# Performance work log

Hardware: AMD Instinct MI355X
Metric: run time of the kernel (lower is better)

## Reference

```python
import jax, jax.numpy as jnp
import numpy as np

HIDDEN = 1024
HEADS = 16
HEAD_DIM = HIDDEN // HEADS


def setup_inputs() -> dict:
    key = jax.random.key(0)
    ks = jax.random.split(key, 9)
    s = 1.0 / np.sqrt(HIDDEN)
    return {
        "x": jax.random.normal(ks[0], (2, 2048, HIDDEN), dtype=jnp.float32),
        "Wq": jax.random.uniform(ks[1], (HIDDEN, HIDDEN), jnp.float32, -s, s),
        "bq": jax.random.uniform(ks[2], (HIDDEN,), jnp.float32, -s, s),
        "Wk": jax.random.uniform(ks[3], (HIDDEN, HIDDEN), jnp.float32, -s, s),
        "bk": jax.random.uniform(ks[4], (HIDDEN,), jnp.float32, -s, s),
        "Wv": jax.random.uniform(ks[5], (HIDDEN, HIDDEN), jnp.float32, -s, s),
        "bv": jax.random.uniform(ks[6], (HIDDEN,), jnp.float32, -s, s),
        "Wo": jax.random.uniform(ks[7], (HIDDEN, HIDDEN), jnp.float32, -s, s),
        "bo": jax.random.uniform(ks[8], (HIDDEN,), jnp.float32, -s, s),
    }


def reference(x, Wq, bq, Wk, bk, Wv, bv, Wo, bo):
    B, N, C = x.shape
    H, D = HEADS, HEAD_DIM
    # torch Linear: y = x @ W.T + b; weights here stored as (out, in)
    q = (x @ Wq.T + bq).reshape(B, N, H, D).transpose(0, 2, 1, 3)  # bhnd
    k = (x @ Wk.T + bk).reshape(B, N, H, D).transpose(0, 2, 1, 3)
    v = (x @ Wv.T + bv).reshape(B, N, H, D).transpose(0, 2, 1, 3)
    scale = D ** -0.5
    attn = jnp.einsum("bhnd,bhmd->bhnm", q, k) * scale
    attn = jax.nn.softmax(attn, axis=-1)
    out = jnp.einsum("bhnm,bhmd->bhnd", attn, v)
    out = out.transpose(0, 2, 1, 3).reshape(B, N, C)
    return out @ Wo.T + bo
```

## Files before the change

### kernel.cpp

```cpp
#include <hip/hip_runtime.h>
#include <stdint.h>

#define HIDDEN 1024
#define HEADS 16
#define HEAD_DIM 64
#define NBATCH 2
#define SEQ 2048

typedef short bh8 __attribute__((ext_vector_type(8)));
typedef _Float16 hf4 __attribute__((ext_vector_type(4)));
typedef _Float16 hf8 __attribute__((ext_vector_type(8)));
typedef float fx4 __attribute__((ext_vector_type(4)));

#define MFMA_BF16(a, b, c) __builtin_amdgcn_mfma_f32_16x16x32_bf16((a), (b), (c), 0, 0, 0)
#define MFMA_F16_16(a, b, c) __builtin_amdgcn_mfma_f32_16x16x16f16((a), (b), (c), 0, 0, 0)

__device__ __forceinline__ short f2bf(float f) {
  union { float f; uint32_t u; } v; v.f = f;
  uint32_t r = v.u + 0x7fffu + ((v.u >> 16) & 1u);
  return (short)(r >> 16);
}
__device__ __forceinline__ short f2h(float f) {
  union { _Float16 h; short s; } v; v.h = (_Float16)f;
  return v.s;
}

typedef __attribute__((address_space(1))) void GV;
typedef __attribute__((address_space(3))) void LV;
__device__ __forceinline__ void gl_lds16(const void* g, void* l) {
  __builtin_amdgcn_global_load_lds((GV*)g, (LV*)l, 16, 0, 0);
}

__device__ __forceinline__ size_t img_off(int row, int k) {
  int rt = row >> 7, kt = k >> 6;
  int g = (((row & 127) >> 4) << 1) + ((k & 63) >> 5);
  int l = (((k & 31) >> 3) << 4) + (row & 15);
  return ((size_t)((rt * 16 + kt) * 16 + g) << 9) + (l << 3) + (k & 7);
}

__global__ void cvt_kernel(const float* __restrict__ x,
                           const float* __restrict__ wq, const float* __restrict__ wk,
                           const float* __restrict__ wv, const float* __restrict__ wo,
                           short* __restrict__ xb, short* __restrict__ wqb,
                           short* __restrict__ wkb, short* __restrict__ wvb,
                           short* __restrict__ wob) {
  long t = (long)blockIdx.x * blockDim.x + threadIdx.x;
  long i = t * 4;
  const float* s; short* d; long off;
  if (i < 4194304L) { s = x; d = xb; off = i; }
  else {
    long j = i - 4194304L;
    int w = (int)(j >> 20);
    off = j & 1048575L;
    s = (w == 0) ? wq : (w == 1) ? wk : (w == 2) ? wv : wo;
    d = (w == 0) ? wqb : (w == 1) ? wkb : (w == 2) ? wvb : wob;
  }
  float4 v = *(const float4*)(s + off);
  short4 o;
  o.x = f2bf(v.x); o.y = f2bf(v.y); o.z = f2bf(v.z); o.w = f2bf(v.w);
  int row = (int)(off >> 10), k = (int)(off & 1023);
  *(short4*)(d + img_off(row, k)) = o;
}

__global__ __launch_bounds__(256)
void qkv_kernel(const short* __restrict__ xb,
                const short* __restrict__ wqb, const short* __restrict__ wkb,
                const short* __restrict__ wvb,
                const float* __restrict__ bq, const float* __restrict__ bk,
                const float* __restrict__ bv,
                short* __restrict__ Q, short* __restrict__ K, short* __restrict__ Vt) {
  __shared__ __align__(16) short Alds[8192];
  __shared__ __align__(16) short Blds[8192];
  const int z = blockIdx.z;
  const short* W = (z == 0) ? wqb : (z == 1) ? wkb : wvb;
  const float* bias = (z == 0) ? bq : (z == 1) ? bk : bv;
  const int mt = blockIdx.y;
  const int ot = blockIdx.x;
  const int tid = threadIdx.x;
  const int lane = tid & 63, w = tid >> 6;
  const int r = lane & 15, q = lane >> 4;
  const int wr = w >> 1, wc = w & 1;

  fx4 acc[4][4] = {};

  for (int kt = 0; kt < 16; ++kt) {
#pragma unroll
    for (int i = 0; i < 4; ++i) {
      int c = w * 4 + i;
      gl_lds16(xb + (((size_t)(mt * 16 + kt) * 16 + c) << 9) + lane * 8,
               (char*)Alds + c * 1024);
      gl_lds16(W + (((size_t)(ot * 16 + kt) * 16 + c) << 9) + lane * 8,
               (char*)Blds + c * 1024);
    }
    __syncthreads();
#pragma unroll
    for (int ks = 0; ks < 2; ++ks) {
      bh8 af[4], bf_[4];
#pragma unroll
      for (int ti = 0; ti < 4; ++ti)
        af[ti] = *(const bh8*)&Alds[(((wr * 4 + ti) * 2 + ks) << 9) + lane * 8];
#pragma unroll
      for (int tj = 0; tj < 4; ++tj)
        bf_[tj] = *(const bh8*)&Blds[(((wc * 4 + tj) * 2 + ks) << 9) + lane * 8];
#pragma unroll
      for (int ti = 0; ti < 4; ++ti)
#pragma unroll
        for (int tj = 0; tj < 4; ++tj)
          acc[ti][tj] = MFMA_BF16(af[ti], bf_[tj], acc[ti][tj]);
    }
    __syncthreads();
  }

  const float QS = 0.18033688011112042f;
#pragma unroll
  for (int ti = 0; ti < 4; ++ti)
#pragma unroll
    for (int tj = 0; tj < 4; ++tj)
#pragma unroll
      for (int i = 0; i < 4; ++i) {
        int row = mt * 128 + wr * 64 + ti * 16 + q * 4 + i;
        int col = ot * 128 + wc * 64 + tj * 16 + r;
        float v = acc[ti][tj][i] + bias[col];
        int b = row >> 11, n = row & 2047;
        int h = col >> 6, d = col & 63;
        int bh = b * 16 + h;
        size_t base = (size_t)bh * 131072;
        if (z == 0) {
          Q[base + (size_t)n * 64 + d] = f2bf(v * QS);
        } else if (z == 1) {
          int jj = n >> 7, rin = n & 127;
          int g = ((rin >> 4) * 2) + (d >> 5);
          int lp = (((d & 31) >> 3) * 16) + (rin & 15);
          K[base + jj * 8192 + g * 512 + lp * 8 + (d & 7)] = f2bf(v);
        } else {
          int jj = n >> 7, keyin = n & 127;
          int dt = d >> 4, rp = d & 15;
          int ks2 = keyin >> 4, pi = ks2 >> 1, hh = ks2 & 1;
          int qp = (keyin & 15) >> 2, ii = keyin & 3;
          Vt[base + jj * 8192 + (dt * 4 + pi) * 512 + (qp * 16 + rp) * 8 + hh * 4 + ii] = f2h(v);
        }
      }
}

__global__ __launch_bounds__(512, 4)
void attn_kernel(const short* __restrict__ Q, const short* __restrict__ Kf,
                 const short* __restrict__ Vf, short* __restrict__ A) {
  __shared__ __align__(16) short Klds[8192];
  __shared__ __align__(16) short Vlds[8192];

  const int tid = threadIdx.x;
  const int lane = tid & 63, w = tid >> 6;
  const int r = lane & 15, q = lane >> 4;
  const int n0 = blockIdx.x * 128;
  const int bh = blockIdx.y;

  const short* Qg = Q + (size_t)bh * 131072;
  const short* Kg = Kf + (size_t)bh * 131072;
  const short* Vg = Vf + (size_t)bh * 131072;

  bh8 qf[2];
#pragma unroll
  for (int ks = 0; ks < 2; ++ks)
    qf[ks] = *(const bh8*)(Qg + (size_t)(n0 + w * 16 + r) * 64 + ks * 32 + q * 8);

  fx4 o[4] = {};
  float l_run = 0.f;

  for (int j = 0; j < 16; ++j) {
    const short* kt = Kg + j * 8192;
    const short* vt = Vg + j * 8192;
#pragma unroll
    for (int i = 0; i < 4; ++i) {
      if (w < 4) {
        int c = w * 4 + i;
        gl_lds16(kt + c * 512 + lane * 8, (char*)Klds + c * 1024);
      } else {
        int c = (w - 4) * 4 + i;
        gl_lds16(vt + c * 512 + lane * 8, (char*)Vlds + c * 1024);
      }
    }
    __syncthreads();

    fx4 s[8] = {};
#pragma unroll
    for (int ks = 0; ks < 2; ++ks)
#pragma unroll
      for (int tj = 0; tj < 8; ++tj) {
        bh8 kf = *(const bh8*)&Klds[(tj * 2 + ks) * 512 + lane * 8];
        s[tj] = MFMA_BF16(kf, qf[ks], s[tj]);
      }

    hf4 p[8];
#pragma unroll
    for (int tj = 0; tj < 8; ++tj)
#pragma unroll
      for (int i = 0; i < 4; ++i) {
        float e = __builtin_amdgcn_exp2f(s[tj][i]);
        l_run += e;
        p[tj][i] = (_Float16)e;
      }

#pragma unroll
    for (int pi = 0; pi < 4; ++pi)
#pragma unroll
      for (int dt = 0; dt < 4; ++dt) {
        hf8 vv = *(const hf8*)&Vlds[(dt * 4 + pi) * 512 + lane * 8];
        hf4 vlo = __builtin_shufflevector(vv, vv, 0, 1, 2, 3);
        hf4 vhi = __builtin_shufflevector(vv, vv, 4, 5, 6, 7);
        o[dt] = MFMA_F16_16(vlo, p[2 * pi], o[dt]);
        o[dt] = MFMA_F16_16(vhi, p[2 * pi + 1], o[dt]);
      }
    __syncthreads();
  }

  float l = l_run;
  l += __shfl_xor(l, 16);
  l += __shfl_xor(l, 32);
  const float inv = 1.0f / l;

  const int h = bh & 15;
  const int mt = (bh >> 4) * 16 + blockIdx.x;
#pragma unroll
  for (int dt = 0; dt < 4; ++dt) {
    short4 ov;
    ov.x = f2bf(o[dt][0] * inv);
    ov.y = f2bf(o[dt][1] * inv);
    ov.z = f2bf(o[dt][2] * inv);
    ov.w = f2bf(o[dt][3] * inv);
    int g = w * 2 + (dt >> 1);
    int lp = ((dt & 1) * 2 + (q >> 1)) * 16 + r;
    *(short4*)(A + (((size_t)(mt * 16 + h) * 16 + g) << 9) + lp * 8 + (q & 1) * 4) = ov;
  }
}

__global__ __launch_bounds__(256)
void proj_kernel(const short* __restrict__ ab, const short* __restrict__ wob,
                 const float* __restrict__ bo, float* __restrict__ out) {
  __shared__ __align__(16) short Alds[8192];
  __shared__ __align__(16) short Blds[8192];
  const int mt = blockIdx.y;
  const int ot = blockIdx.x;
  const int tid = threadIdx.x;
  const int lane = tid & 63, w = tid >> 6;
  const int r = lane & 15, q = lane >> 4;
  const int wr = w >> 1, wc = w & 1;

  fx4 acc[4][4] = {};

  for (int kt = 0; kt < 16; ++kt) {
#pragma unroll
    for (int i = 0; i < 4; ++i) {
      int c = w * 4 + i;
      gl_lds16(ab + (((size_t)(mt * 16 + kt) * 16 + c) << 9) + lane * 8,
               (char*)Alds + c * 1024);
      gl_lds16(wob + (((size_t)(ot * 16 + kt) * 16 + c) << 9) + lane * 8,
               (char*)Blds + c * 1024);
    }
    __syncthreads();
#pragma unroll
    for (int ks = 0; ks < 2; ++ks) {
      bh8 af[4], bf_[4];
#pragma unroll
      for (int ti = 0; ti < 4; ++ti)
        af[ti] = *(const bh8*)&Alds[(((wr * 4 + ti) * 2 + ks) << 9) + lane * 8];
#pragma unroll
      for (int tj = 0; tj < 4; ++tj)
        bf_[tj] = *(const bh8*)&Blds[(((wc * 4 + tj) * 2 + ks) << 9) + lane * 8];
#pragma unroll
      for (int ti = 0; ti < 4; ++ti)
#pragma unroll
        for (int tj = 0; tj < 4; ++tj)
          acc[ti][tj] = MFMA_BF16(af[ti], bf_[tj], acc[ti][tj]);
    }
    __syncthreads();
  }

#pragma unroll
  for (int ti = 0; ti < 4; ++ti)
#pragma unroll
    for (int tj = 0; tj < 4; ++tj)
#pragma unroll
      for (int i = 0; i < 4; ++i) {
        int row = mt * 128 + wr * 64 + ti * 16 + q * 4 + i;
        int col = ot * 128 + wc * 64 + tj * 16 + r;
        out[(size_t)row * 1024 + col] = acc[ti][tj][i] + bo[col];
      }
}

extern "C" void kernel_launch(void* const* d_in, const int* in_sizes, int n_in,
                              void* d_out, int out_size, void* d_ws, size_t ws_size,
                              hipStream_t stream) {
  const float* x  = (const float*)d_in[0];
  const float* Wq = (const float*)d_in[1];
  const float* bq = (const float*)d_in[2];
  const float* Wk = (const float*)d_in[3];
  const float* bk = (const float*)d_in[4];
  const float* Wv = (const float*)d_in[5];
  const float* bv = (const float*)d_in[6];
  const float* Wo = (const float*)d_in[7];
  const float* bo = (const float*)d_in[8];
  float* out = (float*)d_out;
  char* ws = (char*)d_ws;

  short* xb  = (short*)(ws);
  short* wqb = (short*)(ws + 8388608);
  short* wkb = (short*)(ws + 8388608 + 2097152);
  short* wvb = (short*)(ws + 8388608 + 2 * 2097152);
  short* wob = (short*)(ws + 8388608 + 3 * 2097152);
  short* Qb  = (short*)(ws + 16777216);
  short* Kb  = (short*)(ws + 16777216 + 8388608);
  short* Vtb = (short*)(ws + 16777216 + 2 * 8388608);
  short* Ab  = (short*)(ws);

  cvt_kernel<<<8192, 256, 0, stream>>>(x, Wq, Wk, Wv, Wo, xb, wqb, wkb, wvb, wob);
  qkv_kernel<<<dim3(8, 32, 3), 256, 0, stream>>>(xb, wqb, wkb, wvb, bq, bk, bv, Qb, Kb, Vtb);
  attn_kernel<<<dim3(16, 32), 512, 0, stream>>>(Qb, Kb, Vtb, Ab);
  proj_kernel<<<dim3(8, 32), 256, 0, stream>>>(Ab, wob, bo, out);
}
```

Measured before the change: 198.6 us.

## Double-buffer LDS tiles in QKV, attention and projection kernels

Each of the three kernels now keeps two LDS buffers and issues the global-to-LDS loads for the next K-tile (or key/value block) before computing on the current one. This removes one barrier per iteration and is meant to hide global load latency behind MFMA work. In exchange, LDS use per block doubles (64KB in the attention kernel), which can lower how many blocks fit on a CU and cut the latency hiding that occupancy provided.

New measurement: 224.3 us. +12.9%, slower.

```diff
diff --git a/kernel.cpp b/kernel.cpp
--- a/kernel.cpp
+++ b/kernel.cpp
@@ -69,8 +69,8 @@
                 const float* __restrict__ bq, const float* __restrict__ bk,
                 const float* __restrict__ bv,
                 short* __restrict__ Q, short* __restrict__ K, short* __restrict__ Vt) {
-  __shared__ __align__(16) short Alds[8192];
-  __shared__ __align__(16) short Blds[8192];
+  __shared__ __align__(16) short Alds[2][8192];
+  __shared__ __align__(16) short Blds[2][8192];
   const int z = blockIdx.z;
   const short* W = (z == 0) ? wqb : (z == 1) ? wkb : wvb;
   const float* bias = (z == 0) ? bq : (z == 1) ? bk : bv;
@@ -83,25 +83,32 @@
 
   fx4 acc[4][4] = {};
 
+#define QKV_STAGE(kt, b)                                                         \
+  {                                                                              \
+    _Pragma("unroll") for (int i = 0; i < 4; ++i) {                              \
+      int c = w * 4 + i;                                                         \
+      gl_lds16(xb + (((size_t)(mt * 16 + (kt)) * 16 + c) << 9) + lane * 8,       \
+               (char*)&Alds[b][0] + c * 1024);                                   \
+      gl_lds16(W + (((size_t)(ot * 16 + (kt)) * 16 + c) << 9) + lane * 8,        \
+               (char*)&Blds[b][0] + c * 1024);                                   \
+    }                                                                            \
+  }
+
+  QKV_STAGE(0, 0);
+  __syncthreads();
+
   for (int kt = 0; kt < 16; ++kt) {
-#pragma unroll
-    for (int i = 0; i < 4; ++i) {
-      int c = w * 4 + i;
-      gl_lds16(xb + (((size_t)(mt * 16 + kt) * 16 + c) << 9) + lane * 8,
-               (char*)Alds + c * 1024);
-      gl_lds16(W + (((size_t)(ot * 16 + kt) * 16 + c) << 9) + lane * 8,
-               (char*)Blds + c * 1024);
-    }
-    __syncthreads();
+    int cur = kt & 1;
+    if (kt < 15) QKV_STAGE(kt + 1, cur ^ 1);
 #pragma unroll
     for (int ks = 0; ks < 2; ++ks) {
       bh8 af[4], bf_[4];
 #pragma unroll
       for (int ti = 0; ti < 4; ++ti)
-        af[ti] = *(const bh8*)&Alds[(((wr * 4 + ti) * 2 + ks) << 9) + lane * 8];
+        af[ti] = *(const bh8*)&Alds[cur][(((wr * 4 + ti) * 2 + ks) << 9) + lane * 8];
 #pragma unroll
       for (int tj = 0; tj < 4; ++tj)
-        bf_[tj] = *(const bh8*)&Blds[(((wc * 4 + tj) * 2 + ks) << 9) + lane * 8];
+        bf_[tj] = *(const bh8*)&Blds[cur][(((wc * 4 + tj) * 2 + ks) << 9) + lane * 8];
 #pragma unroll
       for (int ti = 0; ti < 4; ++ti)
 #pragma unroll
@@ -110,6 +117,7 @@
     }
     __syncthreads();
   }
+#undef QKV_STAGE
 
   const float QS = 0.18033688011112042f;
 #pragma unroll
@@ -145,8 +153,8 @@
 __global__ __launch_bounds__(512, 4)
 void attn_kernel(const short* __restrict__ Q, const short* __restrict__ Kf,
                  const short* __restrict__ Vf, short* __restrict__ A) {
-  __shared__ __align__(16) short Klds[8192];
-  __shared__ __align__(16) short Vlds[8192];
+  __shared__ __align__(16) short Klds[2][8192];
+  __shared__ __align__(16) short Vlds[2][8192];
 
   const int tid = threadIdx.x;
   const int lane = tid & 63, w = tid >> 6;
@@ -166,27 +174,34 @@
   fx4 o[4] = {};
   float l_run = 0.f;
 
+#define ATTN_STAGE(j, b)                                                        \
+  {                                                                             \
+    const short* ktp = Kg + (j) * 8192;                                         \
+    const short* vtp = Vg + (j) * 8192;                                         \
+    _Pragma("unroll") for (int i = 0; i < 4; ++i) {                             \
+      if (w < 4) {                                                              \
+        int c = w * 4 + i;                                                      \
+        gl_lds16(ktp + c * 512 + lane * 8, (char*)&Klds[b][0] + c * 1024);      \
+      } else {                                                                  \
+        int c = (w - 4) * 4 + i;                                                \
+        gl_lds16(vtp + c * 512 + lane * 8, (char*)&Vlds[b][0] + c * 1024);      \
+      }                                                                         \
+    }                                                                           \
+  }
+
+  ATTN_STAGE(0, 0);
+  __syncthreads();
+
   for (int j = 0; j < 16; ++j) {
-    const short* kt = Kg + j * 8192;
-    const short* vt = Vg + j * 8192;
-#pragma unroll
-    for (int i = 0; i < 4; ++i) {
-      if (w < 4) {
-        int c = w * 4 + i;
-        gl_lds16(kt + c * 512 + lane * 8, (char*)Klds + c * 1024);
-      } else {
-        int c = (w - 4) * 4 + i;
-        gl_lds16(vt + c * 512 + lane * 8, (char*)Vlds + c * 1024);
-      }
-    }
-    __syncthreads();
+    int cur = j & 1;
+    if (j < 15) ATTN_STAGE(j + 1, cur ^ 1);
 
     fx4 s[8] = {};
 #pragma unroll
     for (int ks = 0; ks < 2; ++ks)
 #pragma unroll
       for (int tj = 0; tj < 8; ++tj) {
-        bh8 kf = *(const bh8*)&Klds[(tj * 2 + ks) * 512 + lane * 8];
+        bh8 kf = *(const bh8*)&Klds[cur][(tj * 2 + ks) * 512 + lane * 8];
         s[tj] = MFMA_BF16(kf, qf[ks], s[tj]);
       }
 
@@ -204,7 +219,7 @@
     for (int pi = 0; pi < 4; ++pi)
 #pragma unroll
       for (int dt = 0; dt < 4; ++dt) {
-        hf8 vv = *(const hf8*)&Vlds[(dt * 4 + pi) * 512 + lane * 8];
+        hf8 vv = *(const hf8*)&Vlds[cur][(dt * 4 + pi) * 512 + lane * 8];
         hf4 vlo = __builtin_shufflevector(vv, vv, 0, 1, 2, 3);
         hf4 vhi = __builtin_shufflevector(vv, vv, 4, 5, 6, 7);
         o[dt] = MFMA_F16_16(vlo, p[2 * pi], o[dt]);
@@ -212,6 +227,7 @@
       }
     __syncthreads();
   }
+#undef ATTN_STAGE
 
   float l = l_run;
   l += __shfl_xor(l, 16);
@@ -236,8 +252,8 @@
 __global__ __launch_bounds__(256)
 void proj_kernel(const short* __restrict__ ab, const short* __restrict__ wob,
                  const float* __restrict__ bo, float* __restrict__ out) {
-  __shared__ __align__(16) short Alds[8192];
-  __shared__ __align__(16) short Blds[8192];
+  __shared__ __align__(16) short Alds[2][8192];
+  __shared__ __align__(16) short Blds[2][8192];
   const int mt = blockIdx.y;
   const int ot = blockIdx.x;
   const int tid = threadIdx.x;
@@ -247,25 +263,32 @@
 
   fx4 acc[4][4] = {};
 
+#define PROJ_STAGE(kt, b)                                                        \
+  {                                                                              \
+    _Pragma("unroll") for (int i = 0; i < 4; ++i) {                              \
+      int c = w * 4 + i;                                                         \
+      gl_lds16(ab + (((size_t)(mt * 16 + (kt)) * 16 + c) << 9) + lane * 8,       \
+               (char*)&Alds[b][0] + c * 1024);                                   \
+      gl_lds16(wob + (((size_t)(ot * 16 + (kt)) * 16 + c) << 9) + lane * 8,      \
+               (char*)&Blds[b][0] + c * 1024);                                   \
+    }                                                                            \
+  }
+
+  PROJ_STAGE(0, 0);
+  __syncthreads();
+
   for (int kt = 0; kt < 16; ++kt) {
-#pragma unroll
-    for (int i = 0; i < 4; ++i) {
-      int c = w * 4 + i;
-      gl_lds16(ab + (((size_t)(mt * 16 + kt) * 16 + c) << 9) + lane * 8,
-               (char*)Alds + c * 1024);
-      gl_lds16(wob + (((size_t)(ot * 16 + kt) * 16 + c) << 9) + lane * 8,
-               (char*)Blds + c * 1024);
-    }
-    __syncthreads();
+    int cur = kt & 1;
+    if (kt < 15) PROJ_STAGE(kt + 1, cur ^ 1);
 #pragma unroll
     for (int ks = 0; ks < 2; ++ks) {
       bh8 af[4], bf_[4];
 #pragma unroll
       for (int ti = 0; ti < 4; ++ti)
-        af[ti] = *(const bh8*)&Alds[(((wr * 4 + ti) * 2 + ks) << 9) + lane * 8];
+        af[ti] = *(const bh8*)&Alds[cur][(((wr * 4 + ti) * 2 + ks) << 9) + lane * 8];
 #pragma unroll
       for (int tj = 0; tj < 4; ++tj)
-        bf_[tj] = *(const bh8*)&Blds[(((wc * 4 + tj) * 2 + ks) << 9) + lane * 8];
+        bf_[tj] = *(const bh8*)&Blds[cur][(((wc * 4 + tj) * 2 + ks) << 9) + lane * 8];
 #pragma unroll
       for (int ti = 0; ti < 4; ++ti)
 #pragma unroll
@@ -274,6 +297,7 @@
     }
     __syncthreads();
   }
+#undef PROJ_STAGE
 
 #pragma unroll
   for (int ti = 0; ti < 4; ++ti)
```

## Double-buffer attention K/V tiles and remap block indices for XCD locality

Applied to the files above, without the earlier changes.

The attention kernel now double-buffers its K/V LDS tiles, prefetching the next key block while the current one is computed, so global-to-LDS loads overlap with MFMA work. All three GEMM/attention kernels switch to 1D grids with a manual block-index swizzle that groups blocks sharing input tiles (same rows or same head) onto the same XCD to improve L2 reuse. Double buffering doubles attention LDS to 64KB per block, which may reduce occupancy below the declared 4 blocks per CU.

Measured after the change: 195.7 us. Within noise of the previous version (-1.5%).

```diff
diff --git a/kernel.cpp b/kernel.cpp
--- a/kernel.cpp
+++ b/kernel.cpp
@@ -71,11 +71,15 @@
                 short* __restrict__ Q, short* __restrict__ K, short* __restrict__ Vt) {
   __shared__ __align__(16) short Alds[8192];
   __shared__ __align__(16) short Blds[8192];
-  const int z = blockIdx.z;
+
+  const int lin = blockIdx.x;
+  const int xcd = lin & 7, idx = lin >> 3;
+  const int mt = (xcd >> 1) * 8 + (idx & 7);
+  const int zo = (xcd & 1) * 12 + (idx >> 3);
+  const int z = zo >> 3, ot = zo & 7;
+
   const short* W = (z == 0) ? wqb : (z == 1) ? wkb : wvb;
   const float* bias = (z == 0) ? bq : (z == 1) ? bk : bv;
-  const int mt = blockIdx.y;
-  const int ot = blockIdx.x;
   const int tid = threadIdx.x;
   const int lane = tid & 63, w = tid >> 6;
   const int r = lane & 15, q = lane >> 4;
@@ -145,14 +149,17 @@
 __global__ __launch_bounds__(512, 4)
 void attn_kernel(const short* __restrict__ Q, const short* __restrict__ Kf,
                  const short* __restrict__ Vf, short* __restrict__ A) {
-  __shared__ __align__(16) short Klds[8192];
-  __shared__ __align__(16) short Vlds[8192];
+  __shared__ __align__(16) short Klds[2][8192];
+  __shared__ __align__(16) short Vlds[2][8192];
+
+  const int lin = blockIdx.x;
+  const int xcd = lin & 7, idx = lin >> 3;
+  const int bh = xcd + 8 * (idx & 3);
+  const int n0 = (idx >> 2) * 128;
 
   const int tid = threadIdx.x;
   const int lane = tid & 63, w = tid >> 6;
   const int r = lane & 15, q = lane >> 4;
-  const int n0 = blockIdx.x * 128;
-  const int bh = blockIdx.y;
 
   const short* Qg = Q + (size_t)bh * 131072;
   const short* Kg = Kf + (size_t)bh * 131072;
@@ -166,27 +173,34 @@
   fx4 o[4] = {};
   float l_run = 0.f;
 
+#define ATTN_STAGE(j, b)                                                        \
+  {                                                                             \
+    const short* ktp = Kg + (j) * 8192;                                         \
+    const short* vtp = Vg + (j) * 8192;                                         \
+    _Pragma("unroll") for (int i = 0; i < 4; ++i) {                             \
+      if (w < 4) {                                                              \
+        int c = w * 4 + i;                                                      \
+        gl_lds16(ktp + c * 512 + lane * 8, (char*)&Klds[b][0] + c * 1024);      \
+      } else {                                                                  \
+        int c = (w - 4) * 4 + i;                                                \
+        gl_lds16(vtp + c * 512 + lane * 8, (char*)&Vlds[b][0] + c * 1024);      \
+      }                                                                         \
+    }                                                                           \
+  }
+
+  ATTN_STAGE(0, 0);
+  __syncthreads();
+
   for (int j = 0; j < 16; ++j) {
-    const short* kt = Kg + j * 8192;
-    const short* vt = Vg + j * 8192;
-#pragma unroll
-    for (int i = 0; i < 4; ++i) {
-      if (w < 4) {
-        int c = w * 4 + i;
-        gl_lds16(kt + c * 512 + lane * 8, (char*)Klds + c * 1024);
-      } else {
-        int c = (w - 4) * 4 + i;
-        gl_lds16(vt + c * 512 + lane * 8, (char*)Vlds + c * 1024);
-      }
-    }
-    __syncthreads();
+    int cur = j & 1;
+    if (j < 15) ATTN_STAGE(j + 1, cur ^ 1);
 
     fx4 s[8] = {};
 #pragma unroll
     for (int ks = 0; ks < 2; ++ks)
 #pragma unroll
       for (int tj = 0; tj < 8; ++tj) {
-        bh8 kf = *(const bh8*)&Klds[(tj * 2 + ks) * 512 + lane * 8];
+        bh8 kf = *(const bh8*)&Klds[cur][(tj * 2 + ks) * 512 + lane * 8];
         s[tj] = MFMA_BF16(kf, qf[ks], s[tj]);
       }
 
@@ -204,7 +218,7 @@
     for (int pi = 0; pi < 4; ++pi)
 #pragma unroll
       for (int dt = 0; dt < 4; ++dt) {
-        hf8 vv = *(const hf8*)&Vlds[(dt * 4 + pi) * 512 + lane * 8];
+        hf8 vv = *(const hf8*)&Vlds[cur][(dt * 4 + pi) * 512 + lane * 8];
         hf4 vlo = __builtin_shufflevector(vv, vv, 0, 1, 2, 3);
         hf4 vhi = __builtin_shufflevector(vv, vv, 4, 5, 6, 7);
         o[dt] = MFMA_F16_16(vlo, p[2 * pi], o[dt]);
@@ -212,6 +226,7 @@
       }
     __syncthreads();
   }
+#undef ATTN_STAGE
 
   float l = l_run;
   l += __shfl_xor(l, 16);
@@ -219,7 +234,7 @@
   const float inv = 1.0f / l;
 
   const int h = bh & 15;
-  const int mt = (bh >> 4) * 16 + blockIdx.x;
+  const int mt = (bh >> 4) * 16 + (n0 >> 7);
 #pragma unroll
   for (int dt = 0; dt < 4; ++dt) {
     short4 ov;
@@ -238,8 +253,12 @@
                  const float* __restrict__ bo, float* __restrict__ out) {
   __shared__ __align__(16) short Alds[8192];
   __shared__ __align__(16) short Blds[8192];
-  const int mt = blockIdx.y;
-  const int ot = blockIdx.x;
+
+  const int lin = blockIdx.x;
+  const int xcd = lin & 7, idx = lin >> 3;
+  const int mt = (xcd >> 1) * 8 + (idx & 7);
+  const int ot = (xcd & 1) * 4 + (idx >> 3);
+
   const int tid = threadIdx.x;
   const int lane = tid & 63, w = tid >> 6;
   const int r = lane & 15, q = lane >> 4;
@@ -313,7 +332,7 @@
   short* Ab  = (short*)(ws);
 
   cvt_kernel<<<8192, 256, 0, stream>>>(x, Wq, Wk, Wv, Wo, xb, wqb, wkb, wvb, wob);
-  qkv_kernel<<<dim3(8, 32, 3), 256, 0, stream>>>(xb, wqb, wkb, wvb, bq, bk, bv, Qb, Kb, Vtb);
-  attn_kernel<<<dim3(16, 32), 512, 0, stream>>>(Qb, Kb, Vtb, Ab);
-  proj_kernel<<<dim3(8, 32), 256, 0, stream>>>(Ab, wob, bo, out);
-}
+  qkv_kernel<<<768, 256, 0, stream>>>(xb, wqb, wkb, wvb, bq, bk, bv, Qb, Kb, Vtb);
+  attn_kernel<<<512, 512, 0, stream>>>(Qb, Kb, Vtb, Ab);
+  proj_kernel<<<256, 256, 0, stream>>>(Ab, wob, bo, out);
+}
```
